# Kernel optimization log

Hardware: AMD Instinct MI355X
Metric: run time of the kernel (lower is better)

## Reference

```python
import math
import jax, jax.numpy as jnp
import numpy as np

CHANNELS = 512
OUT_CHANNELS = 512
N_HEADS = 8
K_CHANNELS = CHANNELS // N_HEADS
WINDOW = 4


def _get_relative_embeddings(emb, length):
    # emb: [1, 2*WINDOW+1, d] -> [1, 2*length-1, d]
    max_rel = 2 * WINDOW + 1
    pad_length = max(0, length - (WINDOW + 1))
    start = max(0, WINDOW + 1 - length)
    end = max_rel + 2 * length - 1
    if pad_length > 0:
        emb = jnp.pad(emb, ((0, 0), (pad_length, pad_length), (0, 0)))
    return emb[:, start:end]


def _rel_to_abs(x):
    # x: [b, h, l, 2l-1] -> [b, h, l, l] via skewing trick
    b, h, l, _ = x.shape
    x = jnp.pad(x, ((0, 0), (0, 0), (0, 0), (0, 1)))
    x_flat = x.reshape(b, h, l * 2 * l)
    x_flat = jnp.pad(x_flat, ((0, 0), (0, 0), (0, l - 1)))
    return x_flat.reshape(b, h, l + 1, 2 * l - 1)[..., :l, l - 1:]


def _abs_to_rel(x):
    # x: [b, h, l, l] -> [b, h, l, 2l-1]
    b, h, l, _ = x.shape
    x = jnp.pad(x, ((0, 0), (0, 0), (0, 0), (0, l - 1)))
    x_flat = x.reshape(b, h, -1)
    x_flat = jnp.pad(x_flat, ((0, 0), (0, 0), (l, 0)))
    return x_flat.reshape(b, h, l, 2 * l)[..., 1:]


def setup_inputs() -> dict:
    key = jax.random.key(0)
    ks = jax.random.split(key, 12)
    B, T = 4, 1024
    w_std = 1.0 / math.sqrt(CHANNELS)
    rel_std = K_CHANNELS ** (-0.5)
    return {
        'x': jax.random.normal(ks[0], (B, T, CHANNELS), jnp.float32),
        'c': jax.random.normal(ks[1], (B, T, CHANNELS), jnp.float32),
        'Wq': jax.random.normal(ks[2], (CHANNELS, CHANNELS), jnp.float32) * w_std,
        'bq': jnp.zeros((CHANNELS,), jnp.float32),
        'Wk': jax.random.normal(ks[3], (CHANNELS, CHANNELS), jnp.float32) * w_std,
        'bk': jnp.zeros((CHANNELS,), jnp.float32),
        'Wv': jax.random.normal(ks[4], (CHANNELS, CHANNELS), jnp.float32) * w_std,
        'bv': jnp.zeros((CHANNELS,), jnp.float32),
        'Wo': jax.random.normal(ks[5], (CHANNELS, OUT_CHANNELS), jnp.float32) * w_std,
        'bo': jnp.zeros((OUT_CHANNELS,), jnp.float32),
        'emb_rel_k': jax.random.normal(ks[6], (1, 2 * WINDOW + 1, K_CHANNELS), jnp.float32) * rel_std,
        'emb_rel_v': jax.random.normal(ks[7], (1, 2 * WINDOW + 1, K_CHANNELS), jnp.float32) * rel_std,
    }


def reference(x, c, Wq, bq, Wk, bk, Wv, bv, Wo, bo, emb_rel_k, emb_rel_v):
    b, t_t, _ = x.shape
    t_s = c.shape[1]
    # 1x1 convs == pointwise dense projections
    q = x @ Wq + bq
    k = c @ Wk + bk
    v = c @ Wv + bv
    q = q.reshape(b, t_t, N_HEADS, K_CHANNELS).transpose(0, 2, 1, 3)
    k = k.reshape(b, t_s, N_HEADS, K_CHANNELS).transpose(0, 2, 1, 3)
    v = v.reshape(b, t_s, N_HEADS, K_CHANNELS).transpose(0, 2, 1, 3)
    q_scaled = q / math.sqrt(K_CHANNELS)
    scores = jnp.einsum('bhtd,bhsd->bhts', q_scaled, k)
    # relative position bias via skewing trick (heads_share=True -> rel emb head dim 1)
    rel_k = _get_relative_embeddings(emb_rel_k, t_s)[0]  # [2*t_s-1, d]
    rel_logits = jnp.einsum('bhtd,md->bhtm', q_scaled, rel_k)
    scores = scores + _rel_to_abs(rel_logits)
    p_attn = jax.nn.softmax(scores, axis=-1)
    out = jnp.einsum('bhts,bhsd->bhtd', p_attn, v)
    rel_w = _abs_to_rel(p_attn)  # [b, h, t, 2t-1]
    rel_v = _get_relative_embeddings(emb_rel_v, t_s)[0]  # [2*t_s-1, d]
    out = out + jnp.einsum('bhtm,md->bhtd', rel_w, rel_v)
    out = out.transpose(0, 2, 1, 3).reshape(b, t_t, CHANNELS)
    return out @ Wo + bo
```

## Files before the change

### kernel.cpp

```cpp
#include <hip/hip_runtime.h>
#include <hip/hip_bf16.h>

#define B_ 4
#define T_ 1024
#define C_ 512
#define H_ 8

typedef __attribute__((ext_vector_type(8))) short short8;
typedef __attribute__((ext_vector_type(4))) float floatx4;

__device__ __forceinline__ unsigned short f2bs(float f) {
    __hip_bfloat16 h = __float2bfloat16(f);
    return *(unsigned short*)&h;
}
__device__ __forceinline__ float bs2f(unsigned short u) {
    __hip_bfloat16 h;
    *(unsigned short*)&h = u;
    return __bfloat162float(h);
}

__device__ __forceinline__ void gload_lds16(const void* g, void* l) {
    __builtin_amdgcn_global_load_lds(
        (const __attribute__((address_space(1))) unsigned int*)g,
        (__attribute__((address_space(3))) unsigned int*)l, 16, 0, 0);
}

__global__ __launch_bounds__(256) void prep(
    const float* __restrict__ Wq, const float* __restrict__ Wk,
    const float* __restrict__ Wv, const float* __restrict__ Wo,
    unsigned short* __restrict__ WT)
{
    __shared__ unsigned short tileT[32][33];
    const int r = blockIdx.x, tid = threadIdx.x;
    const int w = r >> 8, tile = r & 255;
    const int k0 = (tile >> 4) * 32, n0 = (tile & 15) * 32;
    const float* W = (w == 0) ? Wq : (w == 1) ? Wk : (w == 2) ? Wv : Wo;
    unsigned short* out = WT + (size_t)w * 512 * 512;
    const int kk = tid >> 3, ns = (tid & 7) * 4;
    const float4 v = *(const float4*)&W[(size_t)(k0 + kk) * 512 + n0 + ns];
    tileT[ns + 0][kk] = f2bs(v.x);
    tileT[ns + 1][kk] = f2bs(v.y);
    tileT[ns + 2][kk] = f2bs(v.z);
    tileT[ns + 3][kk] = f2bs(v.w);
    __syncthreads();
    const int nn = tid >> 3, ks = (tid & 7) * 4;
    ushort4 o;
    o.x = tileT[nn][ks + 0]; o.y = tileT[nn][ks + 1];
    o.z = tileT[nn][ks + 2]; o.w = tileT[nn][ks + 3];
    *(ushort4*)&out[(size_t)(n0 + nn) * 512 + k0 + ks] = o;
}

__global__ __launch_bounds__(256) void qkv_mfma(
    const float* __restrict__ x, const float* __restrict__ cc,
    const unsigned short* __restrict__ WT,
    const float* __restrict__ bq, const float* __restrict__ bk,
    const float* __restrict__ bv,
    unsigned short* __restrict__ Qc, unsigned short* __restrict__ Kc,
    unsigned short* __restrict__ Vtg)
{
    const int z = blockIdx.z;
    const float* A32 = (z == 0) ? x : cc;
    const unsigned short* Bt = WT + (size_t)z * 262144;
    const float* bias = (z == 0) ? bq : (z == 1) ? bk : bv;
    const float scale = (z == 0) ? 0.125f : 1.0f;

    __shared__ __align__(16) unsigned short sA[2 * 128 * 32];
    __shared__ __align__(16) unsigned short sB[2 * 128 * 32];

    const int tid = threadIdx.x;
    const int wave = tid >> 6, lane = tid & 63;
    const int m0 = blockIdx.y * 128, n0 = blockIdx.x * 128;
    const int mrow = lane & 15, quad = lane >> 4, kgrp = quad * 8;
    const int mhalf = (wave & 1) * 64, noff = (wave >> 1) * 64;
    const int lrow = lane >> 2, lseg = (lane & 3) * 16;

    const int fr0 = tid >> 3;
    const int fc4 = (tid & 7) * 4;

    floatx4 acc[4][4];
    #pragma unroll
    for (int i = 0; i < 4; i++)
        #pragma unroll
        for (int j = 0; j < 4; j++)
            acc[i][j] = (floatx4){0.f, 0.f, 0.f, 0.f};

    float4 a4[4];
    #pragma unroll
    for (int p = 0; p < 4; p++)
        a4[p] = *(const float4*)&A32[(size_t)(m0 + fr0 + p * 32) * 512 + fc4];
    #pragma unroll
    for (int j = 0; j < 2; j++) {
        const int rB = wave * 32 + j * 16 + lrow;
        gload_lds16((const char*)Bt + ((size_t)(n0 + rB) * 512) * 2 + lseg,
                    &sB[(size_t)(wave * 32 + j * 16) * 32]);
    }
    #pragma unroll
    for (int p = 0; p < 4; p++) {
        ushort4 o;
        o.x = f2bs(a4[p].x); o.y = f2bs(a4[p].y);
        o.z = f2bs(a4[p].z); o.w = f2bs(a4[p].w);
        *(ushort4*)&sA[(fr0 + p * 32) * 32 + fc4] = o;
    }

    for (int ck = 0; ck < 16; ck++) {
        const int buf = ck & 1;
        __syncthreads();
        if (ck < 15) {
            const int k0 = (ck + 1) * 32;
            #pragma unroll
            for (int j = 0; j < 2; j++) {
                const int rB = wave * 32 + j * 16 + lrow;
                gload_lds16((const char*)Bt + ((size_t)(n0 + rB) * 512 + k0) * 2 + lseg,
                            &sB[(size_t)((buf ^ 1) * 128 + wave * 32 + j * 16) * 32]);
            }
            #pragma unroll
            for (int p = 0; p < 4; p++)
                a4[p] = *(const float4*)&A32[(size_t)(m0 + fr0 + p * 32) * 512 + k0 + fc4];
        }
        const unsigned short* sAb = sA + (size_t)buf * 128 * 32;
        const unsigned short* sBb = sB + (size_t)buf * 128 * 32;
        short8 af[4], bfv[4];
        #pragma unroll
        for (int i = 0; i < 4; i++)
            af[i] = *(const short8*)&sAb[(size_t)(mhalf + i * 16 + mrow) * 32 + kgrp];
        #pragma unroll
        for (int i = 0; i < 4; i++)
            bfv[i] = *(const short8*)&sBb[(size_t)(noff + i * 16 + mrow) * 32 + kgrp];
        #pragma unroll
        for (int mt = 0; mt < 4; mt++)
            #pragma unroll
            for (int nt = 0; nt < 4; nt++)
                acc[mt][nt] = __builtin_amdgcn_mfma_f32_16x16x32_bf16(
                    af[mt], bfv[nt], acc[mt][nt], 0, 0, 0);
        if (ck < 15) {
            unsigned short* dst = sA + (size_t)(buf ^ 1) * 128 * 32;
            #pragma unroll
            for (int p = 0; p < 4; p++) {
                ushort4 o;
                o.x = f2bs(a4[p].x); o.y = f2bs(a4[p].y);
                o.z = f2bs(a4[p].z); o.w = f2bs(a4[p].w);
                *(ushort4*)&dst[(fr0 + p * 32) * 32 + fc4] = o;
            }
        }
    }

    const int rowq = quad * 4;
    if (z < 2) {
        unsigned short* Y = (z == 0) ? Qc : Kc;
        #pragma unroll
        for (int nt = 0; nt < 4; nt++) {
            const int n = n0 + noff + nt * 16 + mrow;
            const float bv_ = bias[n];
            const int h = n >> 6, d = n & 63;
            #pragma unroll
            for (int mt = 0; mt < 4; mt++)
                #pragma unroll
                for (int r = 0; r < 4; r++) {
                    const int m = m0 + mhalf + mt * 16 + rowq + r;
                    const int bb = m >> 10, t = m & 1023;
                    Y[(((size_t)bb * H_ + h) * 1024 + t) * 64 + d] =
                        f2bs((acc[mt][nt][r] + bv_) * scale);
                }
        }
    } else {
        #pragma unroll
        for (int nt = 0; nt < 4; nt++) {
            const int n = n0 + noff + nt * 16 + mrow;
            const float bv_ = bias[n];
            const int h = n >> 6, d = n & 63;
            #pragma unroll
            for (int mt = 0; mt < 4; mt++) {
                const int m = m0 + mhalf + mt * 16 + rowq;
                const int bb = m >> 10, t = m & 1023;
                ushort4 o4;
                o4.x = f2bs(acc[mt][nt][0] + bv_);
                o4.y = f2bs(acc[mt][nt][1] + bv_);
                o4.z = f2bs(acc[mt][nt][2] + bv_);
                o4.w = f2bs(acc[mt][nt][3] + bv_);
                *(ushort4*)&Vtg[(((size_t)bb * H_ + h) * 64 + d) * 1024 + t] = o4;
            }
        }
    }
}

__global__ __launch_bounds__(256) void out_mfma(
    const unsigned short* __restrict__ AOb, const unsigned short* __restrict__ WoT,
    const float* __restrict__ bias, float* __restrict__ out)
{
    __shared__ __align__(16) unsigned short sA[2 * 128 * 32];
    __shared__ __align__(16) unsigned short sB[2 * 64 * 32];

    const int tid = threadIdx.x;
    const int wave = tid >> 6, lane = tid & 63;
    const int m0 = blockIdx.y * 128, n0 = blockIdx.x * 64;
    const int mrow = lane & 15, quad = lane >> 4, kgrp = quad * 8;
    const int mhalf = (wave & 1) * 64, noff = (wave >> 1) * 32;
    const int lrow = lane >> 2, lseg = (lane & 3) * 16;

    floatx4 acc[4][2];
    #pragma unroll
    for (int i = 0; i < 4; i++)
        #pragma unroll
        for (int j = 0; j < 2; j++)
            acc[i][j] = (floatx4){0.f, 0.f, 0.f, 0.f};

    auto stage = [&](int k0, int bufi) {
        #pragma unroll
        for (int j = 0; j < 2; j++) {
            const int rA = wave * 32 + j * 16 + lrow;
            gload_lds16((const char*)AOb + ((size_t)(m0 + rA) * 512 + k0) * 2 + lseg,
                        &sA[(size_t)(bufi * 128 + wave * 32 + j * 16) * 32]);
        }
        const int rB = wave * 16 + lrow;
        gload_lds16((const char*)WoT + ((size_t)(n0 + rB) * 512 + k0) * 2 + lseg,
                    &sB[(size_t)(bufi * 64 + wave * 16) * 32]);
    };

    stage(0, 0);
    for (int ck = 0; ck < 16; ck++) {
        const int buf = ck & 1;
        __syncthreads();
        if (ck < 15) stage((ck + 1) * 32, buf ^ 1);
        const unsigned short* sAb = sA + (size_t)buf * 128 * 32;
        const unsigned short* sBb = sB + (size_t)buf * 64 * 32;
        short8 af[4], bfv[2];
        #pragma unroll
        for (int i = 0; i < 4; i++)
            af[i] = *(const short8*)&sAb[(size_t)(mhalf + i * 16 + mrow) * 32 + kgrp];
        #pragma unroll
        for (int i = 0; i < 2; i++)
            bfv[i] = *(const short8*)&sBb[(size_t)(noff + i * 16 + mrow) * 32 + kgrp];
        #pragma unroll
        for (int mt = 0; mt < 4; mt++)
            #pragma unroll
            for (int nt = 0; nt < 2; nt++)
                acc[mt][nt] = __builtin_amdgcn_mfma_f32_16x16x32_bf16(
                    af[mt], bfv[nt], acc[mt][nt], 0, 0, 0);
    }

    const int rowq = quad * 4;
    #pragma unroll
    for (int nt = 0; nt < 2; nt++) {
        const int n = n0 + noff + nt * 16 + mrow;
        const float bv_ = bias[n];
        #pragma unroll
        for (int mt = 0; mt < 4; mt++)
            #pragma unroll
            for (int r = 0; r < 4; r++) {
                const int m = m0 + mhalf + mt * 16 + rowq + r;
                out[(size_t)m * 512 + n] = acc[mt][nt][r] + bv_;
            }
    }
}

__device__ __forceinline__ void attn_stage(
    const unsigned short* __restrict__ Kc, const unsigned short* __restrict__ Vtg,
    size_t qkbase, size_t vtbase, int s0, int wave, int ldrow, int gseg,
    unsigned short* KLb, unsigned short* VtLb)
{
    #pragma unroll
    for (int j = 0; j < 2; j++) {
        const int br = wave * 16 + j * 8;
        gload_lds16((const char*)Kc + (qkbase + (size_t)(s0 + br + ldrow) * 64) * 2 + gseg * 16,
                    &KLb[br * 64]);
        gload_lds16((const char*)Vtg + (vtbase + (size_t)(br + ldrow) * 1024 + s0) * 2 + gseg * 16,
                    &VtLb[br * 64]);
    }
}

__global__ __launch_bounds__(256) void attn_mfma(
    const unsigned short* __restrict__ Qc, const unsigned short* __restrict__ Kc,
    const unsigned short* __restrict__ Vtg,
    const float* __restrict__ rk, const float* __restrict__ rv,
    unsigned short* __restrict__ AOb)
{
    __shared__ __align__(16) unsigned short KL[2][64 * 64];
    __shared__ __align__(16) unsigned short VtL[2][64 * 64];
    __shared__ __align__(16) unsigned short PL[4][16 * 72];
    __shared__ float qbL[64 * 9];
    __shared__ float bandL[64 * 9];
    __shared__ float rvL[9 * 64];
    __shared__ float lL[64];

    const int tb = blockIdx.x, bh = blockIdx.y;
    const int b = bh >> 3, h = bh & 7;
    const int tid = threadIdx.x;
    const int wave = tid >> 6, lane = tid & 63;
    const int t0 = tb * 64;
    const int t0w = t0 + wave * 16;
    const size_t qkbase = (size_t)bh * T_ * 64;
    const size_t vtbase = (size_t)bh * 64 * T_;

    const int mrow = lane & 15;
    const int quad = lane >> 4;
    const int kgrp = quad * 8;
    const int x7 = mrow & 7;
    const int ldrow = lane >> 3;
    const int gseg = (lane & 7) ^ ldrow;

    attn_stage(Kc, Vtg, qkbase, vtbase, 0, wave, ldrow, gseg, &KL[0][0], &VtL[0][0]);

    for (int idx = tid; idx < 576; idx += 256) {
        bandL[idx] = 0.f;
        rvL[idx] = rv[idx];
        const int row = idx / 9, w = idx - row * 9;
        const unsigned short* qp = &Qc[qkbase + (size_t)(t0 + row) * 64];
        float s0a = 0.f, s1a = 0.f, s2a = 0.f, s3a = 0.f;
        #pragma unroll
        for (int d8 = 0; d8 < 8; d8 += 4) {
            const short8 q0 = *(const short8*)&qp[d8 * 8];
            const short8 q1 = *(const short8*)&qp[(d8 + 1) * 8];
            const short8 q2 = *(const short8*)&qp[(d8 + 2) * 8];
            const short8 q3 = *(const short8*)&qp[(d8 + 3) * 8];
            #pragma unroll
            for (int i = 0; i < 8; i++) {
                s0a = fmaf(bs2f((unsigned short)q0[i]), rk[w * 64 + d8 * 8 + i], s0a);
                s1a = fmaf(bs2f((unsigned short)q1[i]), rk[w * 64 + (d8 + 1) * 8 + i], s1a);
                s2a = fmaf(bs2f((unsigned short)q2[i]), rk[w * 64 + (d8 + 2) * 8 + i], s2a);
                s3a = fmaf(bs2f((unsigned short)q3[i]), rk[w * 64 + (d8 + 3) * 8 + i], s3a);
            }
        }
        qbL[idx] = (s0a + s1a) + (s2a + s3a);
    }

    const short8 aQ0 = *(const short8*)&Qc[qkbase + (size_t)(t0w + mrow) * 64 + kgrp];
    const short8 aQ1 = *(const short8*)&Qc[qkbase + (size_t)(t0w + mrow) * 64 + 32 + kgrp];

    floatx4 Oc[4];
    float lsA[4] = {0.f, 0.f, 0.f, 0.f};
    #pragma unroll
    for (int dt = 0; dt < 4; dt++) Oc[dt] = (floatx4){0.f, 0.f, 0.f, 0.f};

    unsigned short* Pw = &PL[wave][0];
    float* qbw = &qbL[wave * 16 * 9];
    float* bandw = &bandL[wave * 16 * 9];

    for (int ck = 0; ck < 16; ck++) {
        const int s0 = ck * 64;
        const int buf = ck & 1;
        __syncthreads();
        if (ck < 15)
            attn_stage(Kc, Vtg, qkbase, vtbase, s0 + 64, wave, ldrow, gseg,
                       &KL[buf ^ 1][0], &VtL[buf ^ 1][0]);

        floatx4 Sc[4];
        #pragma unroll
        for (int st = 0; st < 4; st++) {
            const int row = st * 16 + mrow;
            const short8 aK0 = *(const short8*)&KL[buf][row * 64 + (quad ^ x7) * 8];
            const short8 aK1 = *(const short8*)&KL[buf][row * 64 + ((4 + quad) ^ x7) * 8];
            floatx4 s4 = {0.f, 0.f, 0.f, 0.f};
            s4 = __builtin_amdgcn_mfma_f32_16x16x32_bf16(aK0, aQ0, s4, 0, 0, 0);
            s4 = __builtin_amdgcn_mfma_f32_16x16x32_bf16(aK1, aQ1, s4, 0, 0, 0);
            Sc[st] = s4;
        }

        #pragma unroll
        for (int st = 0; st < 4; st++) {
            const int diff = s0 + st * 16 - t0w;
            float p0, p1, p2, p3;
            if (diff >= -19 && diff <= 19) {
                #pragma unroll
                for (int r = 0; r < 4; r++) {
                    const int rel = diff + quad * 4 + r - mrow;
                    float sc = Sc[st][r];
                    const bool inband = (rel >= -4) && (rel <= 4);
                    if (inband) sc += qbw[mrow * 9 + rel + 4];
                    const float p = __expf(sc);
                    if (inband) bandw[mrow * 9 + rel + 4] = p;
                    Sc[st][r] = p;
                }
            } else {
                #pragma unroll
                for (int r = 0; r < 4; r++) Sc[st][r] = __expf(Sc[st][r]);
            }
            p0 = Sc[st][0]; p1 = Sc[st][1]; p2 = Sc[st][2]; p3 = Sc[st][3];
            lsA[st] += (p0 + p1) + (p2 + p3);
            ushort4 o4;
            o4.x = f2bs(p0); o4.y = f2bs(p1); o4.z = f2bs(p2); o4.w = f2bs(p3);
            *(ushort4*)&Pw[mrow * 72 + st * 16 + quad * 4] = o4;
        }

        #pragma unroll
        for (int c = 0; c < 2; c++) {
            const short8 aP = *(const short8*)&Pw[mrow * 72 + c * 32 + kgrp];
            #pragma unroll
            for (int dt = 0; dt < 4; dt++) {
                const int segl = (c * 4 + quad) ^ x7;
                const short8 bV = *(const short8*)&VtL[buf][(dt * 16 + mrow) * 64 + segl * 8];
                Oc[dt] = __builtin_amdgcn_mfma_f32_16x16x32_bf16(aP, bV, Oc[dt], 0, 0, 0);
            }
        }
    }

    float lv = (lsA[0] + lsA[1]) + (lsA[2] + lsA[3]);
    lv += __shfl_xor(lv, 16);
    lv += __shfl_xor(lv, 32);
    if (quad == 0) lL[wave * 16 + mrow] = lv;

    #pragma unroll
    for (int r = 0; r < 4; r++) {
        const int tl = quad * 4 + r;
        const float inv = 1.f / lL[wave * 16 + tl];
        #pragma unroll
        for (int w = 0; w < 9; w++) {
            const float p = bandw[tl * 9 + w];
            #pragma unroll
            for (int dt = 0; dt < 4; dt++)
                Oc[dt][r] = fmaf(p, rvL[w * 64 + dt * 16 + mrow], Oc[dt][r]);
        }
        const int t = t0w + tl;
        #pragma unroll
        for (int dt = 0; dt < 4; dt++)
            AOb[((size_t)b * 1024 + t) * 512 + h * 64 + dt * 16 + mrow] =
                f2bs(Oc[dt][r] * inv);
    }
}

extern "C" void kernel_launch(void* const* d_in, const int* in_sizes, int n_in,
                              void* d_out, int out_size, void* d_ws, size_t ws_size,
                              hipStream_t stream)
{
    const float* x  = (const float*)d_in[0];
    const float* c  = (const float*)d_in[1];
    const float* Wq = (const float*)d_in[2];
    const float* bq = (const float*)d_in[3];
    const float* Wk = (const float*)d_in[4];
    const float* bk = (const float*)d_in[5];
    const float* Wv = (const float*)d_in[6];
    const float* bv = (const float*)d_in[7];
    const float* Wo = (const float*)d_in[8];
    const float* bo = (const float*)d_in[9];
    const float* rk = (const float*)d_in[10];
    const float* rv = (const float*)d_in[11];

    unsigned short* WT  = (unsigned short*)d_ws;
    unsigned short* Qc  = WT + (size_t)4 * 512 * 512;
    unsigned short* Kc  = Qc + (size_t)32 * 1024 * 64;
    unsigned short* Vtg = Kc + (size_t)32 * 1024 * 64;
    unsigned short* AOb = Vtg + (size_t)32 * 1024 * 64;

    prep<<<1024, 256, 0, stream>>>(Wq, Wk, Wv, Wo, WT);
    qkv_mfma<<<dim3(4, 32, 3), 256, 0, stream>>>(x, c, WT, bq, bk, bv, Qc, Kc, Vtg);
    attn_mfma<<<dim3(16, 32), 256, 0, stream>>>(Qc, Kc, Vtg, rk, rv, AOb);
    out_mfma<<<dim3(8, 32), 256, 0, stream>>>(AOb, WT + (size_t)3 * 262144, bo, (float*)d_out);
}
```

Before: 154.1 us.

## Pre-convert activations to bf16 and use exp2 with log2e-folded Q scale

The prep kernel now also converts x and c to bf16 buffers. The QKV GEMM can then stage both operands with direct global-to-LDS loads instead of register fp32 loads and in-loop conversion. The Q scale folds in log2(e) so attention can use the hardware exp2 instead of __expf. This adds an extra write and read of bf16 activations in exchange for simpler, asynchronous GEMM staging and fewer bytes read per GEMM tile.

```diff
diff --git a/kernel.cpp b/kernel.cpp
--- a/kernel.cpp
+++ b/kernel.cpp
@@ -28,30 +28,47 @@
 __global__ __launch_bounds__(256) void prep(
     const float* __restrict__ Wq, const float* __restrict__ Wk,
     const float* __restrict__ Wv, const float* __restrict__ Wo,
-    unsigned short* __restrict__ WT)
+    const float* __restrict__ x, const float* __restrict__ cc,
+    unsigned short* __restrict__ WT,
+    unsigned short* __restrict__ Xb, unsigned short* __restrict__ Cb)
 {
     __shared__ unsigned short tileT[32][33];
     const int r = blockIdx.x, tid = threadIdx.x;
-    const int w = r >> 8, tile = r & 255;
-    const int k0 = (tile >> 4) * 32, n0 = (tile & 15) * 32;
-    const float* W = (w == 0) ? Wq : (w == 1) ? Wk : (w == 2) ? Wv : Wo;
-    unsigned short* out = WT + (size_t)w * 512 * 512;
-    const int kk = tid >> 3, ns = (tid & 7) * 4;
-    const float4 v = *(const float4*)&W[(size_t)(k0 + kk) * 512 + n0 + ns];
-    tileT[ns + 0][kk] = f2bs(v.x);
-    tileT[ns + 1][kk] = f2bs(v.y);
-    tileT[ns + 2][kk] = f2bs(v.z);
-    tileT[ns + 3][kk] = f2bs(v.w);
-    __syncthreads();
-    const int nn = tid >> 3, ks = (tid & 7) * 4;
-    ushort4 o;
-    o.x = tileT[nn][ks + 0]; o.y = tileT[nn][ks + 1];
-    o.z = tileT[nn][ks + 2]; o.w = tileT[nn][ks + 3];
-    *(ushort4*)&out[(size_t)(n0 + nn) * 512 + k0 + ks] = o;
+    if (r < 1024) {
+        const int w = r >> 8, tile = r & 255;
+        const int k0 = (tile >> 4) * 32, n0 = (tile & 15) * 32;
+        const float* W = (w == 0) ? Wq : (w == 1) ? Wk : (w == 2) ? Wv : Wo;
+        unsigned short* out = WT + (size_t)w * 512 * 512;
+        const int kk = tid >> 3, ns = (tid & 7) * 4;
+        const float4 v = *(const float4*)&W[(size_t)(k0 + kk) * 512 + n0 + ns];
+        tileT[ns + 0][kk] = f2bs(v.x);
+        tileT[ns + 1][kk] = f2bs(v.y);
+        tileT[ns + 2][kk] = f2bs(v.z);
+        tileT[ns + 3][kk] = f2bs(v.w);
+        __syncthreads();
+        const int nn = tid >> 3, ks = (tid & 7) * 4;
+        ushort4 o;
+        o.x = tileT[nn][ks + 0]; o.y = tileT[nn][ks + 1];
+        o.z = tileT[nn][ks + 2]; o.w = tileT[nn][ks + 3];
+        *(ushort4*)&out[(size_t)(n0 + nn) * 512 + k0 + ks] = o;
+    } else {
+        const int bi = r - 1024;
+        const bool isx = bi < 1024;
+        const float* src = isx ? x : cc;
+        unsigned short* dst = isx ? Xb : Cb;
+        const int gid = ((bi & 1023) * 256 + tid) * 8;
+        const float4 v0 = *(const float4*)&src[gid];
+        const float4 v1 = *(const float4*)&src[gid + 4];
+        ushort4 a, b;
+        a.x = f2bs(v0.x); a.y = f2bs(v0.y); a.z = f2bs(v0.z); a.w = f2bs(v0.w);
+        b.x = f2bs(v1.x); b.y = f2bs(v1.y); b.z = f2bs(v1.z); b.w = f2bs(v1.w);
+        *(ushort4*)&dst[gid] = a;
+        *(ushort4*)&dst[gid + 4] = b;
+    }
 }
 
 __global__ __launch_bounds__(256) void qkv_mfma(
-    const float* __restrict__ x, const float* __restrict__ cc,
+    const unsigned short* __restrict__ Xb, const unsigned short* __restrict__ Cb,
     const unsigned short* __restrict__ WT,
     const float* __restrict__ bq, const float* __restrict__ bk,
     const float* __restrict__ bv,
@@ -59,10 +76,10 @@
     unsigned short* __restrict__ Vtg)
 {
     const int z = blockIdx.z;
-    const float* A32 = (z == 0) ? x : cc;
+    const unsigned short* Ab = (z == 0) ? Xb : Cb;
     const unsigned short* Bt = WT + (size_t)z * 262144;
     const float* bias = (z == 0) ? bq : (z == 1) ? bk : bv;
-    const float scale = (z == 0) ? 0.125f : 1.0f;
+    const float scale = (z == 0) ? 0.18033688011112042f  : 1.0f;
 
     __shared__ __align__(16) unsigned short sA[2 * 128 * 32];
     __shared__ __align__(16) unsigned short sB[2 * 128 * 32];
@@ -74,9 +91,6 @@
     const int mhalf = (wave & 1) * 64, noff = (wave >> 1) * 64;
     const int lrow = lane >> 2, lseg = (lane & 3) * 16;
 
-    const int fr0 = tid >> 3;
-    const int fc4 = (tid & 7) * 4;
-
     floatx4 acc[4][4];
     #pragma unroll
     for (int i = 0; i < 4; i++)
@@ -84,39 +98,22 @@
         for (int j = 0; j < 4; j++)
             acc[i][j] = (floatx4){0.f, 0.f, 0.f, 0.f};
 
-    float4 a4[4];
-    #pragma unroll
-    for (int p = 0; p < 4; p++)
-        a4[p] = *(const float4*)&A32[(size_t)(m0 + fr0 + p * 32) * 512 + fc4];
-    #pragma unroll
-    for (int j = 0; j < 2; j++) {
-        const int rB = wave * 32 + j * 16 + lrow;
-        gload_lds16((const char*)Bt + ((size_t)(n0 + rB) * 512) * 2 + lseg,
-                    &sB[(size_t)(wave * 32 + j * 16) * 32]);
-    }
-    #pragma unroll
-    for (int p = 0; p < 4; p++) {
-        ushort4 o;
-        o.x = f2bs(a4[p].x); o.y = f2bs(a4[p].y);
-        o.z = f2bs(a4[p].z); o.w = f2bs(a4[p].w);
-        *(ushort4*)&sA[(fr0 + p * 32) * 32 + fc4] = o;
-    }
-
+    auto stage = [&](int k0, int bufi) {
+        #pragma unroll
+        for (int j = 0; j < 2; j++) {
+            const int rr = wave * 32 + j * 16 + lrow;
+            gload_lds16((const char*)Ab + ((size_t)(m0 + rr) * 512 + k0) * 2 + lseg,
+                        &sA[(size_t)(bufi * 128 + wave * 32 + j * 16) * 32]);
+            gload_lds16((const char*)Bt + ((size_t)(n0 + rr) * 512 + k0) * 2 + lseg,
+                        &sB[(size_t)(bufi * 128 + wave * 32 + j * 16) * 32]);
+        }
+    };
+
+    stage(0, 0);
     for (int ck = 0; ck < 16; ck++) {
         const int buf = ck & 1;
         __syncthreads();
-        if (ck < 15) {
-            const int k0 = (ck + 1) * 32;
-            #pragma unroll
-            for (int j = 0; j < 2; j++) {
-                const int rB = wave * 32 + j * 16 + lrow;
-                gload_lds16((const char*)Bt + ((size_t)(n0 + rB) * 512 + k0) * 2 + lseg,
-                            &sB[(size_t)((buf ^ 1) * 128 + wave * 32 + j * 16) * 32]);
-            }
-            #pragma unroll
-            for (int p = 0; p < 4; p++)
-                a4[p] = *(const float4*)&A32[(size_t)(m0 + fr0 + p * 32) * 512 + k0 + fc4];
-        }
+        if (ck < 15) stage((ck + 1) * 32, buf ^ 1);
         const unsigned short* sAb = sA + (size_t)buf * 128 * 32;
         const unsigned short* sBb = sB + (size_t)buf * 128 * 32;
         short8 af[4], bfv[4];
@@ -132,16 +129,6 @@
             for (int nt = 0; nt < 4; nt++)
                 acc[mt][nt] = __builtin_amdgcn_mfma_f32_16x16x32_bf16(
                     af[mt], bfv[nt], acc[mt][nt], 0, 0, 0);
-        if (ck < 15) {
-            unsigned short* dst = sA + (size_t)(buf ^ 1) * 128 * 32;
-            #pragma unroll
-            for (int p = 0; p < 4; p++) {
-                ushort4 o;
-                o.x = f2bs(a4[p].x); o.y = f2bs(a4[p].y);
-                o.z = f2bs(a4[p].z); o.w = f2bs(a4[p].w);
-                *(ushort4*)&dst[(fr0 + p * 32) * 32 + fc4] = o;
-            }
-        }
     }
 
     const int rowq = quad * 4;
@@ -366,13 +353,14 @@
                     float sc = Sc[st][r];
                     const bool inband = (rel >= -4) && (rel <= 4);
                     if (inband) sc += qbw[mrow * 9 + rel + 4];
-                    const float p = __expf(sc);
+                    const float p = __builtin_amdgcn_exp2f(sc);
                     if (inband) bandw[mrow * 9 + rel + 4] = p;
                     Sc[st][r] = p;
                 }
             } else {
                 #pragma unroll
-                for (int r = 0; r < 4; r++) Sc[st][r] = __expf(Sc[st][r]);
+                for (int r = 0; r < 4; r++)
+                    Sc[st][r] = __builtin_amdgcn_exp2f(Sc[st][r]);
             }
             p0 = Sc[st][0]; p1 = Sc[st][1]; p2 = Sc[st][2]; p3 = Sc[st][3];
             lsA[st] += (p0 + p1) + (p2 + p3);
@@ -439,9 +427,11 @@
     unsigned short* Kc  = Qc + (size_t)32 * 1024 * 64;
     unsigned short* Vtg = Kc + (size_t)32 * 1024 * 64;
     unsigned short* AOb = Vtg + (size_t)32 * 1024 * 64;
-
-    prep<<<1024, 256, 0, stream>>>(Wq, Wk, Wv, Wo, WT);
-    qkv_mfma<<<dim3(4, 32, 3), 256, 0, stream>>>(x, c, WT, bq, bk, bv, Qc, Kc, Vtg);
+    unsigned short* Xb  = AOb + (size_t)4096 * 512;
+    unsigned short* Cb  = Xb + (size_t)4096 * 512;
+
+    prep<<<3072, 256, 0, stream>>>(Wq, Wk, Wv, Wo, x, c, WT, Xb, Cb);
+    qkv_mfma<<<dim3(4, 32, 3), 256, 0, stream>>>(Xb, Cb, WT, bq, bk, bv, Qc, Kc, Vtg);
     attn_mfma<<<dim3(16, 32), 256, 0, stream>>>(Qc, Kc, Vtg, rk, rv, AOb);
     out_mfma<<<dim3(8, 32), 256, 0, stream>>>(AOb, WT + (size_t)3 * 262144, bo, (float*)d_out);
 }
```

Measured after the change: 152.2 us. About the same (-1.2%).
